# Performance work log

Measured on AMD Instinct MI355X. Metric: run time of the kernel, lower is better.

## Reference

```python
import jax, jax.numpy as jnp
import numpy as np

N, E, F, H, L, G, O = 100000, 1600000, 128, 128, 4, 512, 10
BN_EPS = 1e-5


def setup_inputs() -> dict:
    key = jax.random.key(0)
    ks = jax.random.split(key, 12)
    x = jax.random.normal(ks[0], (N, F), dtype=jnp.float32)
    edge_index = jax.random.randint(ks[1], (2, E), 0, N, dtype=jnp.int32)
    batch = jnp.sort(jax.random.randint(ks[2], (N,), 0, G, dtype=jnp.int32))
    s = 1.0 / np.sqrt(H)
    # 4 GIN layers, input_dim == hidden_dim so params stack uniformly
    W1s = jax.random.uniform(ks[3], (L, F, H), jnp.float32, -s, s)
    b1s = jnp.zeros((L, H), jnp.float32)
    W2s = jax.random.uniform(ks[4], (L, H, H), jnp.float32, -s, s)
    b2s = jnp.zeros((L, H), jnp.float32)
    eps = jnp.zeros((L,), jnp.float32)  # learnable eps, init 0
    gammas = jnp.ones((L, H), jnp.float32)
    betas = jnp.zeros((L, H), jnp.float32)
    Din = F + L * H  # concatenated graph embedding dim
    so = 1.0 / np.sqrt(Din)
    Wout = jax.random.uniform(ks[5], (Din, O), jnp.float32, -so, so)
    bout = jnp.zeros((O,), jnp.float32)
    return {"x": x, "edge_index": edge_index, "batch": batch,
            "W1s": W1s, "b1s": b1s, "W2s": W2s, "b2s": b2s, "eps": eps,
            "gammas": gammas, "betas": betas, "Wout": Wout, "bout": bout}


def reference(x, edge_index, batch, W1s, b1s, W2s, b2s, eps, gammas, betas, Wout, bout):
    src, dst = edge_index[0], edge_index[1]
    n = x.shape[0]
    pooled = [jax.ops.segment_sum(x, batch, num_segments=G)]  # [G, F]
    h = x
    for l in range(W1s.shape[0]):
        # GINConv: MLP((1+eps)*h + sum_{j in N(i)} h_j)
        agg = jax.ops.segment_sum(h[src], dst, num_segments=n)  # [N, H]
        z = (1.0 + eps[l]) * h + agg
        z = jax.nn.relu(z @ W1s[l] + b1s[l]) @ W2s[l] + b2s[l]
        # BatchNorm1d (batch statistics, biased variance) + ReLU; dropout=identity (eval)
        mu = z.mean(axis=0)
        var = z.var(axis=0)
        z = (z - mu) * jax.lax.rsqrt(var + BN_EPS) * gammas[l] + betas[l]
        h = jax.nn.relu(z)
        pooled.append(jax.ops.segment_sum(h, batch, num_segments=G))  # [G, H]
    emb = jnp.concatenate(pooled, axis=1)  # [G, F + L*H]
    return emb @ Wout + bout  # [G, O]
```

## Files before the change

### kernel.cpp

```cpp
#include <hip/hip_runtime.h>
#include <hip/hip_bf16.h>

typedef __attribute__((ext_vector_type(8))) __bf16 bf16x8;
typedef __attribute__((ext_vector_type(4))) float f32x4;
typedef unsigned short u16;
typedef unsigned int u32;

constexpr int Nn = 100000;
constexpr int Ee = 1600000;
constexpr int Hd = 128;
constexpr int Ll = 4;
constexpr int Gg = 512;
constexpr int Oo = 10;
constexpr int Din = Hd + Ll * Hd;
constexpr int SPLIT = 8;
constexpr int NBLK = (Nn + 127) / 128;

constexpr int NB = 256;
constexpr int NPB = 392;
constexpr int BCAP = 8192;
constexpr int BATCH = 8192;
constexpr int NBATCH = (Ee + BATCH - 1) / BATCH;

__device__ __forceinline__ int swzb(int row, int bc) {
  return (row << 8) + (bc ^ ((row & 7) << 4));
}

__device__ __forceinline__ u16 f2bf(float f) {
  __hip_bfloat16 b = __float2bfloat16(f);
  u16 u;
  __builtin_memcpy(&u, &b, 2);
  return u;
}

__device__ __forceinline__ float bf2f(u32 u) { return __uint_as_float(u << 16); }

__device__ __forceinline__ int lower_bound_dev(const int* a, int n, int key) {
  int lo = 0, hi = n;
  while (lo < hi) { int mid = (lo + hi) >> 1; if (a[mid] < key) lo = mid + 1; else hi = mid; }
  return lo;
}

__global__ __launch_bounds__(256) void xcvt_kernel(const float* __restrict__ x, __hip_bfloat16* __restrict__ xb) {
  int i = blockIdx.x * 256 + threadIdx.x;
  const int total = Nn * Hd / 8;
  if (i >= total) return;
  f32x4 v0 = *(const f32x4*)(x + (size_t)i * 8);
  f32x4 v1 = *(const f32x4*)(x + (size_t)i * 8 + 4);
  uint4 o;
  o.x = (u32)f2bf(v0[0]) | ((u32)f2bf(v0[1]) << 16);
  o.y = (u32)f2bf(v0[2]) | ((u32)f2bf(v0[3]) << 16);
  o.z = (u32)f2bf(v1[0]) | ((u32)f2bf(v1[1]) << 16);
  o.w = (u32)f2bf(v1[2]) | ((u32)f2bf(v1[3]) << 16);
  *(uint4*)((u16*)xb + (size_t)i * 8) = o;
}

__global__ __launch_bounds__(256) void wprep_kernel(const float* __restrict__ W1s,
                                                    const float* __restrict__ W2s,
                                                    __hip_bfloat16* __restrict__ wt) {
  int idx = blockIdx.x * 256 + threadIdx.x;
  if (idx >= Ll * 2 * Hd * Hd) return;
  int l = idx >> 15;
  int w = (idx >> 14) & 1;
  int nn = (idx >> 7) & 127;
  int k = idx & 127;
  const float* W = w ? W2s : W1s;
  wt[idx] = __float2bfloat16(W[l * Hd * Hd + k * Hd + nn]);
}

__global__ void initgptr_kernel(int* __restrict__ gptr) {
  int i = threadIdx.x;
  if (i < NB) gptr[i] = i * BCAP;
}

__global__ __launch_bounds__(256) void binA_kernel(const int* __restrict__ src, const int* __restrict__ dst,
                                                   int* __restrict__ gptr, u32* __restrict__ buckets) {
  __shared__ int hist[NB];
  __shared__ int lbase[NB];
  __shared__ int lpos[NB];
  __shared__ int gbaseS[NB];
  __shared__ int scanT[NB];
  __shared__ u32 reorder[BATCH];
  const int tid = threadIdx.x;
  const int e0 = blockIdx.x * BATCH;
  const int n = min(BATCH, Ee - e0);

  hist[tid] = 0;
  __syncthreads();
  for (int k = tid; k < n; k += 256) {
    int d = dst[e0 + k];
    atomicAdd(&hist[d / NPB], 1);
  }
  __syncthreads();
  int v = hist[tid];
  scanT[tid] = v;
  __syncthreads();
  for (int off = 1; off < NB; off <<= 1) {
    int x = (tid >= off) ? scanT[tid - off] : 0;
    __syncthreads();
    scanT[tid] += x;
    __syncthreads();
  }
  lbase[tid] = scanT[tid] - v;
  lpos[tid] = 0;
  __syncthreads();
  for (int k = tid; k < n; k += 256) {
    int d = dst[e0 + k];
    int s = src[e0 + k];
    int b = d / NPB;
    int dlo = d - b * NPB;
    int p = lbase[b] + atomicAdd(&lpos[b], 1);
    reorder[p] = ((u32)dlo << 17) | (u32)s;
  }
  __syncthreads();
  if (hist[tid] > 0) gbaseS[tid] = atomicAdd(&gptr[tid], hist[tid]);
  __syncthreads();
  for (int p = tid; p < n; p += 256) {
    int lo = 0, hi = NB - 1;
    while (lo < hi) { int mid = (lo + hi + 1) >> 1; if (lbase[mid] <= p) lo = mid; else hi = mid - 1; }
    buckets[gbaseS[lo] + (p - lbase[lo])] = reorder[p];
  }
}

__global__ __launch_bounds__(256) void bucketscan_kernel(const int* __restrict__ gptr,
                                                         int* __restrict__ bmeta,
                                                         int* __restrict__ indptr) {
  __shared__ int sc[NB];
  int tid = threadIdx.x;
  int cnt = gptr[tid] - tid * BCAP;
  sc[tid] = cnt;
  __syncthreads();
  for (int off = 1; off < NB; off <<= 1) {
    int x = (tid >= off) ? sc[tid - off] : 0;
    __syncthreads();
    sc[tid] += x;
    __syncthreads();
  }
  bmeta[tid] = cnt;
  bmeta[NB + tid] = sc[tid] - cnt;
  if (tid == 0) indptr[Nn] = Ee;
}

__global__ __launch_bounds__(512) void place_kernel(const u32* __restrict__ buckets,
                                                    const int* __restrict__ bmeta,
                                                    int* __restrict__ indptr, int* __restrict__ adj) {
  __shared__ int ncnt[512];
  __shared__ int nofs[NPB];
  __shared__ int lcur[NPB];
  const int tid = threadIdx.x;
  const int b = blockIdx.x;
  const int cnt = bmeta[b];
  const int adjbase = bmeta[NB + b];
  const int ebase = b * BCAP;
  const int node0 = b * NPB;
  const int nnodes = min(NPB, Nn - node0);

  ncnt[tid] = 0;
  if (tid < NPB) lcur[tid] = 0;
  __syncthreads();
  for (int k = tid; k < cnt; k += 512) atomicAdd(&ncnt[buckets[ebase + k] >> 17], 1);
  __syncthreads();
  int v = ncnt[tid];
  for (int off = 1; off < 512; off <<= 1) {
    int x = (tid >= off) ? ncnt[tid - off] : 0;
    __syncthreads();
    ncnt[tid] += x;
    __syncthreads();
  }
  if (tid < NPB) nofs[tid] = ncnt[tid] - v;
  __syncthreads();
  if (tid < nnodes) indptr[node0 + tid] = adjbase + nofs[tid];
  for (int k = tid; k < cnt; k += 512) {
    u32 u = buckets[ebase + k];
    int dlo = u >> 17;
    int s = (int)(u & 0x1FFFFu);
    int p = atomicAdd(&lcur[dlo], 1);
    adj[adjbase + nofs[dlo] + p] = s;
  }
}

__global__ __launch_bounds__(256) void agg_kernel(const __hip_bfloat16* __restrict__ hb,
                                                  const int* __restrict__ indptr,
                                                  const int* __restrict__ adj,
                                                  const float* __restrict__ epsp,
                                                  int layer, __hip_bfloat16* __restrict__ t) {
  int wid = blockIdx.x * 4 + (threadIdx.x >> 6);
  if (wid >= Nn) return;
  int lane = threadIdx.x & 63;
  int cb = lane * 2;
  const u16* hp = (const u16*)hb;
  u32 selfu = *(const u32*)(hp + (size_t)wid * Hd + cb);
  float eps1 = 1.0f + epsp[layer];
  int s = __builtin_amdgcn_readfirstlane(indptr[wid]);
  int e = __builtin_amdgcn_readfirstlane(indptr[wid + 1]);
  float a0 = 0.f, a1 = 0.f;
  int p = s;
  for (; p + 4 <= e; p += 4) {
    int n0 = adj[p], n1 = adj[p + 1], n2 = adj[p + 2], n3 = adj[p + 3];
    u32 v0 = *(const u32*)(hp + (size_t)n0 * Hd + cb);
    u32 v1 = *(const u32*)(hp + (size_t)n1 * Hd + cb);
    u32 v2 = *(const u32*)(hp + (size_t)n2 * Hd + cb);
    u32 v3 = *(const u32*)(hp + (size_t)n3 * Hd + cb);
    a0 += bf2f(v0 & 0xffffu) + bf2f(v1 & 0xffffu) + bf2f(v2 & 0xffffu) + bf2f(v3 & 0xffffu);
    a1 += bf2f(v0 >> 16) + bf2f(v1 >> 16) + bf2f(v2 >> 16) + bf2f(v3 >> 16);
  }
  for (; p < e; ++p) {
    u32 v0 = *(const u32*)(hp + (size_t)adj[p] * Hd + cb);
    a0 += bf2f(v0 & 0xffffu);
    a1 += bf2f(v0 >> 16);
  }
  a0 += eps1 * bf2f(selfu & 0xffffu);
  a1 += eps1 * bf2f(selfu >> 16);
  u32 outv = (u32)f2bf(a0) | ((u32)f2bf(a1) << 16);
  *(u32*)((u16*)t + (size_t)wid * Hd + cb) = outv;
}

__global__ __launch_bounds__(256) void mlp_kernel(const __hip_bfloat16* __restrict__ t,
                                                  const __hip_bfloat16* __restrict__ w1t,
                                                  const __hip_bfloat16* __restrict__ w2t,
                                                  const float* __restrict__ b1,
                                                  const float* __restrict__ b2,
                                                  __hip_bfloat16* __restrict__ z,
                                                  float* __restrict__ pstats) {
  __shared__ __align__(16) unsigned char sA[32 * 1024];
  __shared__ __align__(16) unsigned char sW[32 * 1024];
  const int tid = threadIdx.x;
  const int m0 = blockIdx.x * 128;

  for (int c = tid; c < 2048; c += 256) {
    int row = c >> 4, bc = (c & 15) << 4;
    int so = swzb(row, bc);
    *(uint4*)(sW + so) = *(const uint4*)((const unsigned char*)w1t + row * 256 + bc);
    uint4 av = make_uint4(0u, 0u, 0u, 0u);
    int gr = m0 + row;
    if (gr < Nn) av = *(const uint4*)((const unsigned char*)t + (size_t)gr * 256 + bc);
    *(uint4*)(sA + so) = av;
  }
  __syncthreads();

  const int lane = tid & 63;
  const int wave = tid >> 6;
  const int lrow = lane & 15;
  const int lkb = (lane >> 4) << 4;
  const int wm = wave * 32;
  const int crow = (lane >> 4) << 2;

  f32x4 acc[2][8];
  #pragma unroll
  for (int a = 0; a < 2; ++a) {
    #pragma unroll
    for (int b = 0; b < 8; ++b) acc[a][b] = (f32x4){0.f, 0.f, 0.f, 0.f};
  }

  #pragma unroll
  for (int kk = 0; kk < 4; ++kk) {
    const int kb2 = kk * 64 + lkb;
    bf16x8 a0 = *(const bf16x8*)(sA + swzb(wm + lrow, kb2));
    bf16x8 a1 = *(const bf16x8*)(sA + swzb(wm + 16 + lrow, kb2));
    #pragma unroll
    for (int nf = 0; nf < 8; ++nf) {
      bf16x8 bfr = *(const bf16x8*)(sW + swzb(nf * 16 + lrow, kb2));
      acc[0][nf] = __builtin_amdgcn_mfma_f32_16x16x32_bf16(a0, bfr, acc[0][nf], 0, 0, 0);
      acc[1][nf] = __builtin_amdgcn_mfma_f32_16x16x32_bf16(a1, bfr, acc[1][nf], 0, 0, 0);
    }
  }
  __syncthreads();

  for (int c = tid; c < 2048; c += 256) {
    int row = c >> 4, bc = (c & 15) << 4;
    *(uint4*)(sW + swzb(row, bc)) = *(const uint4*)((const unsigned char*)w2t + row * 256 + bc);
  }
  #pragma unroll
  for (int nf = 0; nf < 8; ++nf) {
    const int col = nf * 16 + lrow;
    const float bb = b1[col];
    #pragma unroll
    for (int mf = 0; mf < 2; ++mf) {
      #pragma unroll
      for (int j = 0; j < 4; ++j) {
        float v = acc[mf][nf][j] + bb;
        v = v > 0.f ? v : 0.f;
        int row = wm + mf * 16 + crow + j;
        *(u16*)(sA + swzb(row, col * 2)) = f2bf(v);
      }
    }
  }
  __syncthreads();

  f32x4 acc2[2][8];
  #pragma unroll
  for (int a = 0; a < 2; ++a) {
    #pragma unroll
    for (int b = 0; b < 8; ++b) acc2[a][b] = (f32x4){0.f, 0.f, 0.f, 0.f};
  }
  #pragma unroll
  for (int kk = 0; kk < 4; ++kk) {
    const int kb2 = kk * 64 + lkb;
    bf16x8 a0 = *(const bf16x8*)(sA + swzb(wm + lrow, kb2));
    bf16x8 a1 = *(const bf16x8*)(sA + swzb(wm + 16 + lrow, kb2));
    #pragma unroll
    for (int nf = 0; nf < 8; ++nf) {
      bf16x8 bfr = *(const bf16x8*)(sW + swzb(nf * 16 + lrow, kb2));
      acc2[0][nf] = __builtin_amdgcn_mfma_f32_16x16x32_bf16(a0, bfr, acc2[0][nf], 0, 0, 0);
      acc2[1][nf] = __builtin_amdgcn_mfma_f32_16x16x32_bf16(a1, bfr, acc2[1][nf], 0, 0, 0);
    }
  }
  __syncthreads();

  float* sred = (float*)sA;
  float* qred = (float*)(sA + 2048);
  u16* zp = (u16*)z;
  #pragma unroll
  for (int nf = 0; nf < 8; ++nf) {
    const int col = nf * 16 + lrow;
    const float bb = b2[col];
    float s = 0.f, q = 0.f;
    #pragma unroll
    for (int mf = 0; mf < 2; ++mf) {
      #pragma unroll
      for (int j = 0; j < 4; ++j) {
        int grow = m0 + wm + mf * 16 + crow + j;
        if (grow < Nn) {
          float v = acc2[mf][nf][j] + bb;
          zp[(size_t)grow * Hd + col] = f2bf(v);
          s += v; q += v * v;
        }
      }
    }
    s += __shfl_xor(s, 16, 64); s += __shfl_xor(s, 32, 64);
    q += __shfl_xor(q, 16, 64); q += __shfl_xor(q, 32, 64);
    if (lane < 16) { sred[wave * 128 + col] = s; qred[wave * 128 + col] = q; }
  }
  __syncthreads();
  if (tid < 128) {
    float a = sred[tid] + sred[128 + tid] + sred[256 + tid] + sred[384 + tid];
    pstats[(size_t)blockIdx.x * 256 + tid] = a;
  } else {
    int c = tid - 128;
    float a = qred[c] + qred[128 + c] + qred[256 + c] + qred[384 + c];
    pstats[(size_t)blockIdx.x * 256 + tid] = a;
  }
}

__global__ __launch_bounds__(256) void redstats_kernel(const float* __restrict__ pstats,
                                                       float* __restrict__ stats) {
  __shared__ float red[256];
  int slot = blockIdx.x, t = threadIdx.x;
  float a = 0.f;
  for (int i = t; i < NBLK; i += 256) a += pstats[(size_t)i * 256 + slot];
  red[t] = a;
  __syncthreads();
  for (int o = 128; o > 0; o >>= 1) {
    if (t < o) red[t] += red[t + o];
    __syncthreads();
  }
  if (t == 0) stats[slot] = red[0];
}

__global__ __launch_bounds__(128) void bnparam_kernel(const float* __restrict__ stats,
                                                      const float* __restrict__ gammas,
                                                      const float* __restrict__ betas,
                                                      int layer, float* __restrict__ ss) {
  int f = threadIdx.x;
  const float invn = 1.0f / (float)Nn;
  float mu = stats[f] * invn;
  float var = stats[Hd + f] * invn - mu * mu;
  float sc = gammas[layer * Hd + f] * rsqrtf(var + 1e-5f);
  ss[f] = sc;
  ss[Hd + f] = betas[layer * Hd + f] - mu * sc;
}

__global__ __launch_bounds__(128) void pool_kernel(const __hip_bfloat16* __restrict__ v,
                                                   const int* __restrict__ batch,
                                                   float* __restrict__ emb, int colOff) {
  int g = blockIdx.x / SPLIT, sp = blockIdx.x % SPLIT;
  int f = threadIdx.x;
  int lo = lower_bound_dev(batch, Nn, g);
  int hi = lower_bound_dev(batch, Nn, g + 1);
  int len = hi - lo;
  if (len <= 0) return;
  int chunk = (len + SPLIT - 1) / SPLIT;
  int rs = lo + sp * chunk;
  int re = min(rs + chunk, hi);
  if (rs >= re) return;
  const u16* vp = (const u16*)v;
  float acc = 0.f;
  for (int i = rs; i < re; ++i) acc += bf2f((u32)vp[(size_t)i * Hd + f]);
  atomicAdd(&emb[g * Din + colOff + f], acc);
}

__global__ __launch_bounds__(128) void bn_pool_kernel(const __hip_bfloat16* __restrict__ z,
                                                      const float* __restrict__ ss,
                                                      const int* __restrict__ batch,
                                                      __hip_bfloat16* __restrict__ h,
                                                      float* __restrict__ emb, int colOff) {
  int g = blockIdx.x / SPLIT, sp = blockIdx.x % SPLIT;
  int c2 = (threadIdx.x & 63) * 2;
  int rh = threadIdx.x >> 6;
  float sc0 = ss[c2], sh0 = ss[Hd + c2];
  float sc1 = ss[c2 + 1], sh1 = ss[Hd + c2 + 1];
  int lo = lower_bound_dev(batch, Nn, g);
  int hi = lower_bound_dev(batch, Nn, g + 1);
  int len = hi - lo;
  if (len <= 0) return;
  int chunk = (len + SPLIT - 1) / SPLIT;
  int rs = lo + sp * chunk;
  int re = min(rs + chunk, hi);
  if (rs >= re) return;
  const u16* zp = (const u16*)z;
  u16* hp = (u16*)h;
  float a0 = 0.f, a1 = 0.f;
  for (int i = rs + rh; i < re; i += 2) {
    u32 v = *(const u32*)(zp + (size_t)i * Hd + c2);
    float v0 = bf2f(v & 0xffffu) * sc0 + sh0; v0 = fmaxf(v0, 0.f);
    float v1 = bf2f(v >> 16) * sc1 + sh1; v1 = fmaxf(v1, 0.f);
    *(u32*)(hp + (size_t)i * Hd + c2) = (u32)f2bf(v0) | ((u32)f2bf(v1) << 16);
    a0 += v0; a1 += v1;
  }
  atomicAdd(&emb[g * Din + colOff + c2], a0);
  atomicAdd(&emb[g * Din + colOff + c2 + 1], a1);
}

__global__ __launch_bounds__(64) void out_kernel(const float* __restrict__ emb, const float* __restrict__ Wout,
                                                 const float* __restrict__ bout, float* __restrict__ out) {
  int g = blockIdx.x;
  int lane = threadIdx.x;
  float acc[Oo];
  #pragma unroll
  for (int o = 0; o < Oo; ++o) acc[o] = 0.f;
  for (int d = lane; d < Din; d += 64) {
    float ev = emb[g * Din + d];
    #pragma unroll
    for (int o = 0; o < Oo; ++o) acc[o] += ev * Wout[d * Oo + o];
  }
  #pragma unroll
  for (int off = 32; off > 0; off >>= 1) {
    #pragma unroll
    for (int o = 0; o < Oo; ++o) acc[o] += __shfl_down(acc[o], off, 64);
  }
  if (lane == 0) {
    #pragma unroll
    for (int o = 0; o < Oo; ++o) out[g * Oo + o] = acc[o] + bout[o];
  }
}

extern "C" void kernel_launch(void* const* d_in, const int* in_sizes, int n_in,
                              void* d_out, int out_size, void* d_ws, size_t ws_size,
                              hipStream_t stream) {
  (void)in_sizes; (void)n_in; (void)out_size;
  const float* x = (const float*)d_in[0];
  const int* ei = (const int*)d_in[1];
  const int* src = ei;
  const int* dst = ei + Ee;
  const int* batch = (const int*)d_in[2];
  const float* W1s = (const float*)d_in[3];
  const float* b1s = (const float*)d_in[4];
  const float* W2s = (const float*)d_in[5];
  const float* b2s = (const float*)d_in[6];
  const float* eps = (const float*)d_in[7];
  const float* gammas = (const float*)d_in[8];
  const float* betas = (const float*)d_in[9];
  const float* Wout = (const float*)d_in[10];
  const float* bout = (const float*)d_in[11];
  float* out = (float*)d_out;

  unsigned char* ws = (unsigned char*)d_ws;
  size_t off = 0;
  auto alloc = [&](size_t bytes) -> void* {
    void* p = ws + off;
    off = (off + bytes + 255) & ~size_t(255);
    return p;
  };
  __hip_bfloat16* xb = (__hip_bfloat16*)alloc((size_t)Nn * Hd * 2);
  __hip_bfloat16* h = (__hip_bfloat16*)alloc((size_t)Nn * Hd * 2);
  __hip_bfloat16* z = (__hip_bfloat16*)alloc((size_t)Nn * Hd * 2);
  __hip_bfloat16* t = (__hip_bfloat16*)alloc((size_t)Nn * Hd * 2);
  int* indptr = (int*)alloc((size_t)(Nn + 1) * 4);
  int* adj = (int*)alloc((size_t)Ee * 4);
  u32* buckets = (u32*)alloc((size_t)NB * BCAP * 4);
  int* gptr = (int*)alloc((size_t)NB * 4);
  int* bmeta = (int*)alloc((size_t)2 * NB * 4);
  float* emb = (float*)alloc((size_t)Gg * Din * 4);
  float* pstats = (float*)alloc((size_t)NBLK * 256 * 4);
  float* stats = (float*)alloc(256 * 4);
  float* ss = (float*)alloc(256 * 4);
  __hip_bfloat16* wt = (__hip_bfloat16*)alloc((size_t)Ll * 2 * Hd * Hd * 2);
  if (off > ws_size) return;

  hipMemsetAsync(emb, 0, (size_t)Gg * Din * 4, stream);

  xcvt_kernel<<<(Nn * Hd / 8 + 255) / 256, 256, 0, stream>>>(x, xb);
  wprep_kernel<<<(Ll * 2 * Hd * Hd + 255) / 256, 256, 0, stream>>>(W1s, W2s, wt);

  initgptr_kernel<<<1, NB, 0, stream>>>(gptr);
  binA_kernel<<<NBATCH, 256, 0, stream>>>(src, dst, gptr, buckets);
  bucketscan_kernel<<<1, NB, 0, stream>>>(gptr, bmeta, indptr);
  place_kernel<<<NB, 512, 0, stream>>>(buckets, bmeta, indptr, adj);

  pool_kernel<<<Gg * SPLIT, 128, 0, stream>>>(xb, batch, emb, 0);

  const __hip_bfloat16* hcur = xb;
  for (int l = 0; l < Ll; ++l) {
    agg_kernel<<<(Nn + 3) / 4, 256, 0, stream>>>(hcur, indptr, adj, eps, l, t);
    mlp_kernel<<<NBLK, 256, 0, stream>>>(
        t, wt + (size_t)l * 2 * Hd * Hd, wt + (size_t)l * 2 * Hd * Hd + Hd * Hd,
        b1s + l * Hd, b2s + l * Hd, z, pstats);
    redstats_kernel<<<256, 256, 0, stream>>>(pstats, stats);
    bnparam_kernel<<<1, 128, 0, stream>>>(stats, gammas, betas, l, ss);
    bn_pool_kernel<<<Gg * SPLIT, 128, 0, stream>>>(z, ss, batch, h, emb, Hd + l * Hd);
    hcur = h;
  }

  out_kernel<<<Gg, 64, 0, stream>>>(emb, Wout, bout, out);
}
```

Before: 601.7 us.

## Unroll gather to 16 neighbours, fuse BN stat reduction, vectorize input pooling

The aggregation loop now issues 16 independent neighbour loads before accumulating, with 8/4 tails, to raise memory-level parallelism on the gather. The stats reduction and BN parameter kernels are merged into one kernel per feature, removing a launch per layer and the intermediate stats buffer. The initial pooling kernel reads two bf16 per thread and splits rows across two half-blocks. The wider unroll raises register use and may lower occupancy.

```diff
diff --git a/kernel.cpp b/kernel.cpp
--- a/kernel.cpp
+++ b/kernel.cpp
@@ -195,14 +195,29 @@
   int e = __builtin_amdgcn_readfirstlane(indptr[wid + 1]);
   float a0 = 0.f, a1 = 0.f;
   int p = s;
-  for (; p + 4 <= e; p += 4) {
-    int n0 = adj[p], n1 = adj[p + 1], n2 = adj[p + 2], n3 = adj[p + 3];
-    u32 v0 = *(const u32*)(hp + (size_t)n0 * Hd + cb);
-    u32 v1 = *(const u32*)(hp + (size_t)n1 * Hd + cb);
-    u32 v2 = *(const u32*)(hp + (size_t)n2 * Hd + cb);
-    u32 v3 = *(const u32*)(hp + (size_t)n3 * Hd + cb);
-    a0 += bf2f(v0 & 0xffffu) + bf2f(v1 & 0xffffu) + bf2f(v2 & 0xffffu) + bf2f(v3 & 0xffffu);
-    a1 += bf2f(v0 >> 16) + bf2f(v1 >> 16) + bf2f(v2 >> 16) + bf2f(v3 >> 16);
+  while (p + 16 <= e) {
+    u32 v[16];
+    #pragma unroll
+    for (int j = 0; j < 16; ++j) v[j] = *(const u32*)(hp + (size_t)adj[p + j] * Hd + cb);
+    #pragma unroll
+    for (int j = 0; j < 16; ++j) { a0 += bf2f(v[j] & 0xffffu); a1 += bf2f(v[j] >> 16); }
+    p += 16;
+  }
+  if (p + 8 <= e) {
+    u32 v[8];
+    #pragma unroll
+    for (int j = 0; j < 8; ++j) v[j] = *(const u32*)(hp + (size_t)adj[p + j] * Hd + cb);
+    #pragma unroll
+    for (int j = 0; j < 8; ++j) { a0 += bf2f(v[j] & 0xffffu); a1 += bf2f(v[j] >> 16); }
+    p += 8;
+  }
+  if (p + 4 <= e) {
+    u32 v[4];
+    #pragma unroll
+    for (int j = 0; j < 4; ++j) v[j] = *(const u32*)(hp + (size_t)adj[p + j] * Hd + cb);
+    #pragma unroll
+    for (int j = 0; j < 4; ++j) { a0 += bf2f(v[j] & 0xffffu); a1 += bf2f(v[j] >> 16); }
+    p += 4;
   }
   for (; p < e; ++p) {
     u32 v0 = *(const u32*)(hp + (size_t)adj[p] * Hd + cb);
@@ -342,39 +357,41 @@
   }
 }
 
-__global__ __launch_bounds__(256) void redstats_kernel(const float* __restrict__ pstats,
-                                                       float* __restrict__ stats) {
-  __shared__ float red[256];
-  int slot = blockIdx.x, t = threadIdx.x;
-  float a = 0.f;
-  for (int i = t; i < NBLK; i += 256) a += pstats[(size_t)i * 256 + slot];
-  red[t] = a;
+__global__ __launch_bounds__(256) void stats_bn_kernel(const float* __restrict__ pstats,
+                                                       const float* __restrict__ gammas,
+                                                       const float* __restrict__ betas,
+                                                       int layer, float* __restrict__ ss) {
+  __shared__ float reds[256];
+  __shared__ float redq[256];
+  int f = blockIdx.x;
+  int t = threadIdx.x;
+  float s = 0.f, q = 0.f;
+  for (int i = t; i < NBLK; i += 256) {
+    s += pstats[(size_t)i * 256 + f];
+    q += pstats[(size_t)i * 256 + 128 + f];
+  }
+  reds[t] = s; redq[t] = q;
   __syncthreads();
   for (int o = 128; o > 0; o >>= 1) {
-    if (t < o) red[t] += red[t + o];
-    __syncthreads();
-  }
-  if (t == 0) stats[slot] = red[0];
-}
-
-__global__ __launch_bounds__(128) void bnparam_kernel(const float* __restrict__ stats,
-                                                      const float* __restrict__ gammas,
-                                                      const float* __restrict__ betas,
-                                                      int layer, float* __restrict__ ss) {
-  int f = threadIdx.x;
-  const float invn = 1.0f / (float)Nn;
-  float mu = stats[f] * invn;
-  float var = stats[Hd + f] * invn - mu * mu;
-  float sc = gammas[layer * Hd + f] * rsqrtf(var + 1e-5f);
-  ss[f] = sc;
-  ss[Hd + f] = betas[layer * Hd + f] - mu * sc;
+    if (t < o) { reds[t] += reds[t + o]; redq[t] += redq[t + o]; }
+    __syncthreads();
+  }
+  if (t == 0) {
+    const float invn = 1.0f / (float)Nn;
+    float mu = reds[0] * invn;
+    float var = redq[0] * invn - mu * mu;
+    float sc = gammas[layer * Hd + f] * rsqrtf(var + 1e-5f);
+    ss[f] = sc;
+    ss[Hd + f] = betas[layer * Hd + f] - mu * sc;
+  }
 }
 
 __global__ __launch_bounds__(128) void pool_kernel(const __hip_bfloat16* __restrict__ v,
                                                    const int* __restrict__ batch,
                                                    float* __restrict__ emb, int colOff) {
   int g = blockIdx.x / SPLIT, sp = blockIdx.x % SPLIT;
-  int f = threadIdx.x;
+  int c2 = (threadIdx.x & 63) * 2;
+  int rh = threadIdx.x >> 6;
   int lo = lower_bound_dev(batch, Nn, g);
   int hi = lower_bound_dev(batch, Nn, g + 1);
   int len = hi - lo;
@@ -384,9 +401,14 @@
   int re = min(rs + chunk, hi);
   if (rs >= re) return;
   const u16* vp = (const u16*)v;
-  float acc = 0.f;
-  for (int i = rs; i < re; ++i) acc += bf2f((u32)vp[(size_t)i * Hd + f]);
-  atomicAdd(&emb[g * Din + colOff + f], acc);
+  float a0 = 0.f, a1 = 0.f;
+  for (int i = rs + rh; i < re; i += 2) {
+    u32 u = *(const u32*)(vp + (size_t)i * Hd + c2);
+    a0 += bf2f(u & 0xffffu);
+    a1 += bf2f(u >> 16);
+  }
+  atomicAdd(&emb[g * Din + colOff + c2], a0);
+  atomicAdd(&emb[g * Din + colOff + c2 + 1], a1);
 }
 
 __global__ __launch_bounds__(128) void bn_pool_kernel(const __hip_bfloat16* __restrict__ z,
@@ -482,7 +504,6 @@
   int* bmeta = (int*)alloc((size_t)2 * NB * 4);
   float* emb = (float*)alloc((size_t)Gg * Din * 4);
   float* pstats = (float*)alloc((size_t)NBLK * 256 * 4);
-  float* stats = (float*)alloc(256 * 4);
   float* ss = (float*)alloc(256 * 4);
   __hip_bfloat16* wt = (__hip_bfloat16*)alloc((size_t)Ll * 2 * Hd * Hd * 2);
   if (off > ws_size) return;
@@ -505,8 +526,7 @@
     mlp_kernel<<<NBLK, 256, 0, stream>>>(
         t, wt + (size_t)l * 2 * Hd * Hd, wt + (size_t)l * 2 * Hd * Hd + Hd * Hd,
         b1s + l * Hd, b2s + l * Hd, z, pstats);
-    redstats_kernel<<<256, 256, 0, stream>>>(pstats, stats);
-    bnparam_kernel<<<1, 128, 0, stream>>>(stats, gammas, betas, l, ss);
+    stats_bn_kernel<<<128, 256, 0, stream>>>(pstats, gammas, betas, l, ss);
     bn_pool_kernel<<<Gg * SPLIT, 128, 0, stream>>>(z, ss, batch, h, emb, Hd + l * Hd);
     hcur = h;
   }
```

After: 592.4 us. About the same (-1.5%).
